# Kernel optimization log

Measured on AMD Instinct MI355X. Metric: run time of the kernel, lower is better.

## Reference

```python
import jax, jax.numpy as jnp
import numpy as np

B, T, D, U, M = 64, 512, 256, 512, 64  # batch, seq_len, input_dim, units, memory_size


def setup_inputs() -> dict:
    key = jax.random.key(0)
    ks = jax.random.split(key, 16)
    g = lambda k, s: (jax.random.normal(k, s, dtype=jnp.float32) * 0.05)
    return {
        "x": g(ks[0], (B, T, D)),
        "Wi": g(ks[1], (D, U)), "Ui": g(ks[2], (U, U)), "bi": jnp.zeros((U,), jnp.float32),
        "Wf": g(ks[3], (D, U)), "Uf": g(ks[4], (U, U)), "bf": jnp.ones((U,), jnp.float32),
        "Wo": g(ks[5], (D, U)), "Uo": g(ks[6], (U, U)), "bo": jnp.zeros((U,), jnp.float32),
        "Wc": g(ks[7], (D, U)), "Uc": g(ks[8], (U, U)), "bc": jnp.zeros((U,), jnp.float32),
        "We": g(ks[9], (D, M)), "Ue": g(ks[10], (U, M)), "be": jnp.zeros((M,), jnp.float32),
    }


def reference(x, Wi, Ui, bi, Wf, Uf, bf, Wo, Uo, bo, Wc, Uc, bc, We, Ue, be):
    # Fuse the 5 per-step input/hidden matmuls into single GEMMs (same math).
    Wcat = jnp.concatenate([Wi, Wf, Wo, Wc, We], axis=1)   # [D, 4U+M]
    Ucat = jnp.concatenate([Ui, Uf, Uo, Uc, Ue], axis=1)   # [U, 4U+M]
    bcat = jnp.concatenate([bi, bf, bo, bc, be], axis=0)   # [4U+M]

    def step(carry, x_t):
        h, mem = carry                                      # h:[B,U], mem:[B,M,U]
        z = x_t @ Wcat + h @ Ucat + bcat                    # [B, 4U+M]
        zi, zf, zo, zc, ze = jnp.split(z, [U, 2 * U, 3 * U, 4 * U], axis=-1)
        i = jax.nn.sigmoid(zi)
        f = jax.nn.sigmoid(zf)
        o = jax.nn.sigmoid(zo)
        c_tilde = jnp.tanh(zc)
        e = jax.nn.softmax(ze, axis=-1)                     # [B,M]
        mem_contrib = jnp.einsum('bm,bmu->bu', e, mem)      # softmax-weighted memory read
        c = f * mem_contrib + i * c_tilde
        h_new = o * jnp.tanh(c)
        mem_new = jnp.concatenate([c[:, None, :], mem[:, :-1, :]], axis=1)  # shift-register write
        return (h_new, mem_new), h_new

    h0 = jnp.zeros((B, U), x.dtype)
    m0 = jnp.zeros((B, M, U), x.dtype)
    (_, _), hs = jax.lax.scan(step, (h0, m0), jnp.swapaxes(x, 0, 1))  # hs:[T,B,U]
    return jnp.swapaxes(hs, 0, 1)                           # [B,T,U]
```

## Files before the change

### kernel.cpp

```cpp
#include <hip/hip_runtime.h>

#define Bn   64
#define Tn   512
#define Dn   256
#define Un   512
#define Mn   64
#define NTHR 256
#define GRID 128

#define HB_OFF    5120
#define BP_OFF    70656
#define BPU_SH    1572864
#define BPE_SH    49152
#define XF_OFF    881664
#define XF_U4     1048576
#define WS_NEED_F (XF_OFF + XF_U4*4)

typedef __attribute__((ext_vector_type(8))) short short8;
typedef __attribute__((ext_vector_type(4))) float f32x4;
typedef unsigned long long ull;

union frag8 { short8 s; f32x4 f; uint4 u; };

__device__ __forceinline__ float sigmoidf_(float v) { return 1.0f / (1.0f + __expf(-v)); }
__device__ __forceinline__ float tanhf_(float v) {
    const float e = __expf(2.0f * v);
    return (e - 1.0f) / (e + 1.0f);
}

__device__ __forceinline__ unsigned short f2bf(float f) {
    unsigned u = __float_as_uint(f);
    return (unsigned short)((u + 0x7FFFu + ((u >> 16) & 1u)) >> 16);
}

__device__ __forceinline__ void st_agent_u64(ull* p, ull v) {
    __hip_atomic_store(p, v, __ATOMIC_RELAXED, __HIP_MEMORY_SCOPE_AGENT);
}
__device__ __forceinline__ ull ld_agent_u64(const void* p) {
    return __hip_atomic_load((const ull*)p, __ATOMIC_RELAXED, __HIP_MEMORY_SCOPE_AGENT);
}

template<bool USEXF>
__global__ __launch_bounds__(NTHR, 1) void xlstm_k(
    const float* __restrict__ x,
    const float* __restrict__ bi, const float* __restrict__ bf_,
    const float* __restrict__ bo, const float* __restrict__ bc,
    const float* __restrict__ be,
    float* __restrict__ out, float* __restrict__ ws)
{
    __shared__ unsigned short sA[16 * 776];
    __shared__ float zs[1024];
    __shared__ float zel[16 * 68];
    __shared__ float esm[16 * 68];
    __shared__ float sbe[64];

    ull* hb64 = (ull*)(ws + HB_OFF);
    const unsigned short* BPU = (const unsigned short*)(ws + BP_OFF);
    const unsigned short* BPE = BPU + BPU_SH;
    const uint4* XFp = (const uint4*)(ws + XF_OFF);

    const int tid = threadIdx.x, wg = blockIdx.x;
    const int bt = wg >> 5, r = wg & 31;
    const int b0 = bt << 4, u0 = r << 4;
    const int lane = tid & 63, w = tid >> 6;
    const int quad = lane >> 4, m16 = lane & 15;
    const unsigned short* aBase = sA + m16 * 776 + (quad << 3);
    const uint4* xfb = XFp + ((ull)bt << 18) + lane;

    const int bb = tid >> 4, uu = tid & 15;
    const float bia_i = bi[u0 + uu], bia_f = bf_[u0 + uu];
    const float bia_o = bo[u0 + uu], bia_c = bc[u0 + uu];
    float* outp = out + (ull)((b0 + bb) * Tn) * 512 + u0 + uu;
    const float4* xg = (const float4*)x;

    if (tid < 64) sbe[tid] = be[tid];

    unsigned ch[32];
    #pragma unroll
    for (int j = 0; j < 32; ++j) ch[j] = 0u;

    const short8* Bg = (const short8*)BPU + (r * 4 + w) * 24 * 64 + lane;
    const short8* Be = (const short8*)BPE + w * 24 * 64 + lane;
    frag8 Bfg[24], Bfe[24];
    #pragma unroll
    for (int i = 0; i < 24; ++i) { Bfg[i].s = Bg[i << 6]; Bfe[i].s = Be[i << 6]; }

    frag8 xf[8];
    float4 xv[4];
    if (USEXF) {
        #pragma unroll
        for (int kb = 0; kb < 8; ++kb) xf[kb].u = xfb[kb << 6];
    } else {
        #pragma unroll
        for (int i2 = 0; i2 < 4; ++i2) {
            const int i = (i2 << 8) + tid;
            xv[i2] = xg[(((b0 + (i >> 6)) * Tn) << 6) + (i & 63)];
        }
        #pragma unroll
        for (int i2 = 0; i2 < 4; ++i2) {
            const int i = (i2 << 8) + tid;
            ushort4 o; o.x = f2bf(xv[i2].x); o.y = f2bf(xv[i2].y);
            o.z = f2bf(xv[i2].z); o.w = f2bf(xv[i2].w);
            *(ushort4*)(sA + (i >> 6) * 776 + ((i & 63) << 2)) = o;
        }
        #pragma unroll
        for (int i2 = 0; i2 < 4; ++i2) {
            const int i = (i2 << 8) + tid;
            xv[i2] = xg[(((b0 + (i >> 6)) * Tn + 1) << 6) + (i & 63)];
        }
    }
    __syncthreads();

    for (int t = 0; t < Tn; ++t) {
        #pragma unroll
        for (int i = 0; i < 24; ++i) {
            asm volatile("" : "+a"(Bfg[i].f));
            asm volatile("" : "+a"(Bfe[i].f));
        }

        f32x4 ag0 = {0.f, 0.f, 0.f, 0.f}, ag1 = ag0, ae0 = ag0, ae1 = ag0;
        #pragma unroll
        for (int kb = 0; kb < 8; kb += 2) {
            const short8 a0 = USEXF ? xf[kb].s     : *(const short8*)(aBase + (kb << 5));
            const short8 a1 = USEXF ? xf[kb + 1].s : *(const short8*)(aBase + ((kb + 1) << 5));
            ag0 = __builtin_amdgcn_mfma_f32_16x16x32_bf16(a0, Bfg[kb].s,     ag0, 0, 0, 0);
            ae0 = __builtin_amdgcn_mfma_f32_16x16x32_bf16(a0, Bfe[kb].s,     ae0, 0, 0, 0);
            ag1 = __builtin_amdgcn_mfma_f32_16x16x32_bf16(a1, Bfg[kb + 1].s, ag1, 0, 0, 0);
            ae1 = __builtin_amdgcn_mfma_f32_16x16x32_bf16(a1, Bfe[kb + 1].s, ae1, 0, 0, 0);
        }

        if (USEXF) {
            if (t + 1 < Tn) {
                const uint4* xn = xfb + ((t + 1) << 9);
                #pragma unroll
                for (int kb = 0; kb < 8; ++kb) xf[kb].u = xn[kb << 6];
            }
        }

        const ull* hp = hb64 + ((t & 1) << 14) + (b0 << 8) + tid;
        ull hv[16];
        #pragma unroll
        for (int j = 0; j < 16; ++j) hv[j] = ld_agent_u64(hp + (j << 8));
        {
            const unsigned want = (unsigned)t;
            while (true) {
                bool ok = true;
                #pragma unroll
                for (int j = 0; j < 16; ++j) ok &= ((unsigned)(hv[j] >> 32) == want);
                if (__all(ok)) break;
                __builtin_amdgcn_s_sleep(1);
                #pragma unroll
                for (int j = 0; j < 16; ++j) hv[j] = ld_agent_u64(hp + (j << 8));
            }
        }

        #pragma unroll
        for (int j = 0; j < 16; ++j)
            *(unsigned*)(sA + j * 776 + 256 + (tid << 1)) = (unsigned)hv[j];
        __syncthreads();

        if (!USEXF) {
            if (t + 1 < Tn) {
                #pragma unroll
                for (int i2 = 0; i2 < 4; ++i2) {
                    const int i = (i2 << 8) + tid;
                    ushort4 o; o.x = f2bf(xv[i2].x); o.y = f2bf(xv[i2].y);
                    o.z = f2bf(xv[i2].z); o.w = f2bf(xv[i2].w);
                    *(ushort4*)(sA + (i >> 6) * 776 + ((i & 63) << 2)) = o;
                }
            }
            if (t + 2 < Tn) {
                #pragma unroll
                for (int i2 = 0; i2 < 4; ++i2) {
                    const int i = (i2 << 8) + tid;
                    xv[i2] = xg[(((b0 + (i >> 6)) * Tn + t + 2) << 6) + (i & 63)];
                }
            }
        }

        #pragma unroll
        for (int kb = 8; kb < 24; kb += 2) {
            const short8 a0 = *(const short8*)(aBase + (kb << 5));
            const short8 a1 = *(const short8*)(aBase + ((kb + 1) << 5));
            ag0 = __builtin_amdgcn_mfma_f32_16x16x32_bf16(a0, Bfg[kb].s,     ag0, 0, 0, 0);
            ae0 = __builtin_amdgcn_mfma_f32_16x16x32_bf16(a0, Bfe[kb].s,     ae0, 0, 0, 0);
            ag1 = __builtin_amdgcn_mfma_f32_16x16x32_bf16(a1, Bfg[kb + 1].s, ag1, 0, 0, 0);
            ae1 = __builtin_amdgcn_mfma_f32_16x16x32_bf16(a1, Bfe[kb + 1].s, ae1, 0, 0, 0);
        }

        #pragma unroll
        for (int i = 0; i < 4; ++i) {
            zs[(((quad << 2) + i) * 16 + m16) * 4 + w] = ag0[i] + ag1[i];
            zel[((quad << 2) + i) * 68 + (w << 4) + m16] = ae0[i] + ae1[i];
        }
        __syncthreads();

        {
            const float* zb = zel + bb * 68;
            const int l = uu;
            const float e0 = __expf(zb[l]      + sbe[l]);
            const float e1 = __expf(zb[l + 16] + sbe[l + 16]);
            const float e2 = __expf(zb[l + 32] + sbe[l + 32]);
            const float e3 = __expf(zb[l + 48] + sbe[l + 48]);
            float ssum = (e0 + e1) + (e2 + e3);
            #pragma unroll
            for (int off = 8; off; off >>= 1) ssum += __shfl_xor(ssum, off, 16);
            const float inv = 1.0f / ssum;
            float* st = esm + bb * 68;
            st[l]      = e0 * inv;
            st[l + 16] = e1 * inv;
            st[l + 32] = e2 * inv;
            st[l + 48] = e3 * inv;
        }

        const float4 z4 = *(const float4*)(zs + (tid << 2));
        const float zi = z4.x + bia_i;
        const float zf = z4.y + bia_f;
        const float zo = z4.z + bia_o;
        const float zc = z4.w + bia_c;
        float mcA = 0.f, mcB = 0.f, mcC = 0.f, mcD = 0.f;
        const float4* ef = (const float4*)(esm + bb * 68);
        #pragma unroll
        for (int q = 0; q < 4; ++q) {
            const float4 e4 = ef[q];
            const unsigned c0 = ch[2 * q], c1 = ch[2 * q + 1];
            mcA = fmaf(__uint_as_float(c0 << 16),         e4.x, mcA);
            mcA = fmaf(__uint_as_float(c0 & 0xFFFF0000u), e4.y, mcA);
            mcA = fmaf(__uint_as_float(c1 << 16),         e4.z, mcA);
            mcA = fmaf(__uint_as_float(c1 & 0xFFFF0000u), e4.w, mcA);
        }
        #pragma unroll
        for (int q = 4; q < 8; ++q) {
            const float4 e4 = ef[q];
            const unsigned c0 = ch[2 * q], c1 = ch[2 * q + 1];
            mcB = fmaf(__uint_as_float(c0 << 16),         e4.x, mcB);
            mcB = fmaf(__uint_as_float(c0 & 0xFFFF0000u), e4.y, mcB);
            mcB = fmaf(__uint_as_float(c1 << 16),         e4.z, mcB);
            mcB = fmaf(__uint_as_float(c1 & 0xFFFF0000u), e4.w, mcB);
        }
        #pragma unroll
        for (int q = 8; q < 12; ++q) {
            const float4 e4 = ef[q];
            const unsigned c0 = ch[2 * q], c1 = ch[2 * q + 1];
            mcC = fmaf(__uint_as_float(c0 << 16),         e4.x, mcC);
            mcC = fmaf(__uint_as_float(c0 & 0xFFFF0000u), e4.y, mcC);
            mcC = fmaf(__uint_as_float(c1 << 16),         e4.z, mcC);
            mcC = fmaf(__uint_as_float(c1 & 0xFFFF0000u), e4.w, mcC);
        }
        #pragma unroll
        for (int q = 12; q < 16; ++q) {
            const float4 e4 = ef[q];
            const unsigned c0 = ch[2 * q], c1 = ch[2 * q + 1];
            mcD = fmaf(__uint_as_float(c0 << 16),         e4.x, mcD);
            mcD = fmaf(__uint_as_float(c0 & 0xFFFF0000u), e4.y, mcD);
            mcD = fmaf(__uint_as_float(c1 << 16),         e4.z, mcD);
            mcD = fmaf(__uint_as_float(c1 & 0xFFFF0000u), e4.w, mcD);
        }
        const float mc = (mcA + mcB) + (mcC + mcD);
        const float cc = sigmoidf_(zf) * mc + sigmoidf_(zi) * tanhf_(zc);
        const float hh = sigmoidf_(zo) * tanhf_(cc);
        const float nh = __shfl_xor(hh, 1);
        if (!(tid & 1)) {
            const ull v = ((ull)(unsigned)(t + 1) << 32)
                        | (ull)((unsigned)f2bf(hh) | ((unsigned)f2bf(nh) << 16));
            st_agent_u64(hb64 + (((t + 1) & 1) << 14) + ((b0 + bb) << 8)
                         + ((u0 + uu) >> 1), v);
        }
        outp[t << 9] = hh;

        #pragma unroll
        for (int j = 31; j > 0; --j) ch[j] = (ch[j] << 16) | (ch[j - 1] >> 16);
        ch[0] = (ch[0] << 16) | (unsigned)f2bf(cc);
    }
}

__global__ __launch_bounds__(NTHR) void init_k(
    const float* __restrict__ x,
    const float* __restrict__ Wi, const float* __restrict__ Ui,
    const float* __restrict__ Wf, const float* __restrict__ Uf,
    const float* __restrict__ Wo, const float* __restrict__ Uo,
    const float* __restrict__ Wc, const float* __restrict__ Uc,
    const float* __restrict__ We, const float* __restrict__ Ue,
    float* __restrict__ ws, int fillxf)
{
    const int idx = blockIdx.x * NTHR + threadIdx.x;
    const int stride = gridDim.x * NTHR;
    unsigned* ctr = (unsigned*)ws;
    for (int i = idx; i < 512; i += stride) ctr[i] = 0u;
    unsigned* hbu = (unsigned*)(ws + HB_OFF);
    for (int i = idx; i < 65536; i += stride) hbu[i] = 0u;

    unsigned short* BPU = (unsigned short*)(ws + BP_OFF);
    unsigned short* BPE = BPU + BPU_SH;
    const float* Wg[4] = {Wi, Wf, Wo, Wc};
    const float* Ug[4] = {Ui, Uf, Uo, Uc};
    for (int g = idx; g < 196608; g += stride) {
        const int lane = g & 63, rest = g >> 6;
        const int kb = rest % 24, rest2 = rest / 24;
        const int w2 = rest2 & 3, rr = rest2 >> 2;
        const int cs = (rr << 4) + (lane & 15);
        const int kbase = (kb << 5) + ((lane >> 4) << 3);
        #pragma unroll
        for (int j = 0; j < 8; ++j) {
            const int k = kbase + j;
            const float v = (k < 256) ? Wg[w2][(k << 9) + cs]
                                      : Ug[w2][((k - 256) << 9) + cs];
            BPU[(g << 3) + j] = f2bf(v);
        }
    }
    for (int g = idx; g < 6144; g += stride) {
        const int lane = g & 63, rest = g >> 6;
        const int kb = rest % 24, w2 = rest / 24;
        const int cs = (w2 << 4) + (lane & 15);
        const int kbase = (kb << 5) + ((lane >> 4) << 3);
        #pragma unroll
        for (int j = 0; j < 8; ++j) {
            const int k = kbase + j;
            const float v = (k < 256) ? We[(k << 6) + cs] : Ue[((k - 256) << 6) + cs];
            BPE[(g << 3) + j] = f2bf(v);
        }
    }
    if (fillxf) {
        uint4* XFp = (uint4*)(ws + XF_OFF);
        for (int g = idx; g < XF_U4; g += stride) {
            const int lane = g & 63, kb = (g >> 6) & 7, t = (g >> 9) & 511, bt = g >> 18;
            const int m16 = lane & 15, quad = lane >> 4;
            const int b = (bt << 4) + m16;
            const int k0 = (kb << 5) + (quad << 3);
            const float* xr = x + (((ull)(b * Tn + t)) << 8) + k0;
            unsigned short us[8];
            #pragma unroll
            for (int j = 0; j < 8; ++j) us[j] = f2bf(xr[j]);
            uint4 o;
            o.x = (unsigned)us[0] | ((unsigned)us[1] << 16);
            o.y = (unsigned)us[2] | ((unsigned)us[3] << 16);
            o.z = (unsigned)us[4] | ((unsigned)us[5] << 16);
            o.w = (unsigned)us[6] | ((unsigned)us[7] << 16);
            XFp[g] = o;
        }
    }
}

extern "C" void kernel_launch(void* const* d_in, const int* in_sizes, int n_in,
                              void* d_out, int out_size, void* d_ws, size_t ws_size,
                              hipStream_t stream) {
    const float* x  = (const float*)d_in[0];
    const float* Wi = (const float*)d_in[1];
    const float* Ui = (const float*)d_in[2];
    const float* bi = (const float*)d_in[3];
    const float* Wf = (const float*)d_in[4];
    const float* Uf = (const float*)d_in[5];
    const float* bf = (const float*)d_in[6];
    const float* Wo = (const float*)d_in[7];
    const float* Uo = (const float*)d_in[8];
    const float* bo = (const float*)d_in[9];
    const float* Wc = (const float*)d_in[10];
    const float* Uc = (const float*)d_in[11];
    const float* bc = (const float*)d_in[12];
    const float* We = (const float*)d_in[13];
    const float* Ue = (const float*)d_in[14];
    const float* be = (const float*)d_in[15];
    float* out = (float*)d_out;
    float* ws  = (float*)d_ws;

    const int use_xf = (ws_size >= (size_t)WS_NEED_F * sizeof(float)) ? 1 : 0;

    init_k<<<512, NTHR, 0, stream>>>(x, Wi, Ui, Wf, Uf, Wo, Uo, Wc, Uc, We, Ue,
                                     ws, use_xf);

    void* args[] = { &x, &bi, &bf, &bo, &bc, &be, &out, &ws };
    const void* kfun = use_xf ? (const void*)xlstm_k<true>
                              : (const void*)xlstm_k<false>;
    hipError_t e = hipLaunchCooperativeKernel(kfun, dim3(GRID), dim3(NTHR),
                                              args, 0, stream);
    if (e != hipSuccess) {
        (void)hipGetLastError();
        if (use_xf)
            xlstm_k<true><<<GRID, NTHR, 0, stream>>>(x, bi, bf, bo, bc, be, out, ws);
        else
            xlstm_k<false><<<GRID, NTHR, 0, stream>>>(x, bi, bf, bo, bc, be, out, ws);
    }
}
```

Measured before the change: 1.693 ms.

## Interleave two batch tiles per workgroup to hide recurrent sync latency

Adds a dual kernel in which each of 64 workgroups handles two independent 16-row batch tiles. While one tile waits on other workgroups' hidden-state flags, the other tile's input-projection MFMAs and gate math run. This is meant to hide the cross-workgroup spin-wait latency of the serial recurrence. In exchange, half as many CUs are used, and each workgroup does twice the per-step work and carries twice the register state (two memory shift registers and two x fragment sets).

After: 3.065 ms. 81.0% more time.

```diff
diff --git a/kernel.cpp b/kernel.cpp
--- a/kernel.cpp
+++ b/kernel.cpp
@@ -6,7 +6,8 @@
 #define Un   512
 #define Mn   64
 #define NTHR 256
-#define GRID 128
+#define GRID_DUAL 64
+#define GRID_SNG  128
 
 #define HB_OFF    5120
 #define BP_OFF    70656
@@ -40,7 +41,314 @@
     return __hip_atomic_load((const ull*)p, __ATOMIC_RELAXED, __HIP_MEMORY_SCOPE_AGENT);
 }
 
-template<bool USEXF>
+__global__ __launch_bounds__(NTHR, 1) void xlstm_dual(
+    const float* __restrict__ bi, const float* __restrict__ bf_,
+    const float* __restrict__ bo, const float* __restrict__ bc,
+    const float* __restrict__ be,
+    float* __restrict__ out, float* __restrict__ ws)
+{
+    __shared__ unsigned short sH[16 * 520];
+    __shared__ float zs[1024];
+    __shared__ float zel[16 * 68];
+    __shared__ float esm[16 * 68];
+    __shared__ float sbe[64];
+
+    ull* hb64 = (ull*)(ws + HB_OFF);
+    const unsigned short* BPU = (const unsigned short*)(ws + BP_OFF);
+    const unsigned short* BPE = BPU + BPU_SH;
+    const uint4* XFp = (const uint4*)(ws + XF_OFF);
+
+    const int tid = threadIdx.x, wg = blockIdx.x;
+    const int r = wg & 31, pr = wg >> 5;
+    const int btA = pr, btB = pr + 2;
+    const int b0A = btA << 4, b0B = btB << 4, u0 = r << 4;
+    const int lane = tid & 63, w = tid >> 6;
+    const int quad = lane >> 4, m16 = lane & 15;
+    const unsigned short* aBase = sH + m16 * 520 + (quad << 3);
+    const uint4* xfbA = XFp + ((ull)btA << 18) + lane;
+    const uint4* xfbB = XFp + ((ull)btB << 18) + lane;
+
+    const int bb = tid >> 4, uu = tid & 15;
+    const float bia_i = bi[u0 + uu], bia_f = bf_[u0 + uu];
+    const float bia_o = bo[u0 + uu], bia_c = bc[u0 + uu];
+    float* outpA = out + (ull)((b0A + bb) * Tn) * 512 + u0 + uu;
+    float* outpB = out + (ull)((b0B + bb) * Tn) * 512 + u0 + uu;
+
+    if (tid < 64) sbe[tid] = be[tid];
+
+    unsigned chA[32], chB[32];
+    #pragma unroll
+    for (int j = 0; j < 32; ++j) { chA[j] = 0u; chB[j] = 0u; }
+
+    const short8* Bg = (const short8*)BPU + (r * 4 + w) * 24 * 64 + lane;
+    const short8* Be = (const short8*)BPE + w * 24 * 64 + lane;
+    frag8 Bfg[24], Bfe[24];
+    #pragma unroll
+    for (int i = 0; i < 24; ++i) { Bfg[i].s = Bg[i << 6]; Bfe[i].s = Be[i << 6]; }
+
+    frag8 xfA[8], xfB[8];
+    #pragma unroll
+    for (int kb = 0; kb < 8; ++kb) { xfA[kb].u = xfbA[kb << 6]; xfB[kb].u = xfbB[kb << 6]; }
+
+    ull hv[16];
+    {
+        const ull* hp = hb64 + (b0A << 8) + tid;
+        #pragma unroll
+        for (int j = 0; j < 16; ++j) hv[j] = ld_agent_u64(hp + (j << 8));
+    }
+    __syncthreads();
+
+    for (int t = 0; t < Tn; ++t) {
+        #pragma unroll
+        for (int i = 0; i < 24; ++i) {
+            asm volatile("" : "+a"(Bfg[i].f));
+            asm volatile("" : "+a"(Bfe[i].f));
+        }
+        const unsigned want = (unsigned)t;
+        const ull* hpA = hb64 + ((t & 1) << 14) + (b0A << 8) + tid;
+        const ull* hpB = hb64 + ((t & 1) << 14) + (b0B << 8) + tid;
+
+        f32x4 agA0 = {0.f,0.f,0.f,0.f}, agA1 = agA0, aeA0 = agA0, aeA1 = agA0;
+        f32x4 agB0 = agA0, agB1 = agA0, aeB0 = agA0, aeB1 = agA0;
+        #pragma unroll
+        for (int kb = 0; kb < 8; kb += 2) {
+            agA0 = __builtin_amdgcn_mfma_f32_16x16x32_bf16(xfA[kb].s,     Bfg[kb].s,     agA0, 0, 0, 0);
+            aeA0 = __builtin_amdgcn_mfma_f32_16x16x32_bf16(xfA[kb].s,     Bfe[kb].s,     aeA0, 0, 0, 0);
+            agA1 = __builtin_amdgcn_mfma_f32_16x16x32_bf16(xfA[kb + 1].s, Bfg[kb + 1].s, agA1, 0, 0, 0);
+            aeA1 = __builtin_amdgcn_mfma_f32_16x16x32_bf16(xfA[kb + 1].s, Bfe[kb + 1].s, aeA1, 0, 0, 0);
+        }
+        #pragma unroll
+        for (int kb = 0; kb < 8; kb += 2) {
+            agB0 = __builtin_amdgcn_mfma_f32_16x16x32_bf16(xfB[kb].s,     Bfg[kb].s,     agB0, 0, 0, 0);
+            aeB0 = __builtin_amdgcn_mfma_f32_16x16x32_bf16(xfB[kb].s,     Bfe[kb].s,     aeB0, 0, 0, 0);
+            agB1 = __builtin_amdgcn_mfma_f32_16x16x32_bf16(xfB[kb + 1].s, Bfg[kb + 1].s, agB1, 0, 0, 0);
+            aeB1 = __builtin_amdgcn_mfma_f32_16x16x32_bf16(xfB[kb + 1].s, Bfe[kb + 1].s, aeB1, 0, 0, 0);
+        }
+
+        while (true) {
+            bool ok = true;
+            #pragma unroll
+            for (int j = 0; j < 16; ++j) ok &= ((unsigned)(hv[j] >> 32) == want);
+            if (__all(ok)) break;
+            __builtin_amdgcn_s_sleep(1);
+            #pragma unroll
+            for (int j = 0; j < 16; ++j) hv[j] = ld_agent_u64(hpA + (j << 8));
+        }
+        #pragma unroll
+        for (int j = 0; j < 16; ++j)
+            *(unsigned*)(sH + j * 520 + (tid << 1)) = (unsigned)hv[j];
+        __syncthreads();
+
+        #pragma unroll
+        for (int j = 0; j < 16; ++j) hv[j] = ld_agent_u64(hpB + (j << 8));
+
+        #pragma unroll
+        for (int kb = 8; kb < 24; kb += 2) {
+            const short8 a0 = *(const short8*)(aBase + ((kb - 8) << 5));
+            const short8 a1 = *(const short8*)(aBase + ((kb - 7) << 5));
+            agA0 = __builtin_amdgcn_mfma_f32_16x16x32_bf16(a0, Bfg[kb].s,     agA0, 0, 0, 0);
+            aeA0 = __builtin_amdgcn_mfma_f32_16x16x32_bf16(a0, Bfe[kb].s,     aeA0, 0, 0, 0);
+            agA1 = __builtin_amdgcn_mfma_f32_16x16x32_bf16(a1, Bfg[kb + 1].s, agA1, 0, 0, 0);
+            aeA1 = __builtin_amdgcn_mfma_f32_16x16x32_bf16(a1, Bfe[kb + 1].s, aeA1, 0, 0, 0);
+        }
+        #pragma unroll
+        for (int i = 0; i < 4; ++i) {
+            zs[(((quad << 2) + i) * 16 + m16) * 4 + w] = agA0[i] + agA1[i];
+            zel[((quad << 2) + i) * 68 + (w << 4) + m16] = aeA0[i] + aeA1[i];
+        }
+        __syncthreads();
+
+        {
+            const float* zb = zel + bb * 68;
+            const int l = uu;
+            const float e0 = __expf(zb[l]      + sbe[l]);
+            const float e1 = __expf(zb[l + 16] + sbe[l + 16]);
+            const float e2 = __expf(zb[l + 32] + sbe[l + 32]);
+            const float e3 = __expf(zb[l + 48] + sbe[l + 48]);
+            float ssum = (e0 + e1) + (e2 + e3);
+            #pragma unroll
+            for (int off = 8; off; off >>= 1) ssum += __shfl_xor(ssum, off, 16);
+            const float inv = 1.0f / ssum;
+            float* st = esm + bb * 68;
+            st[l] = e0 * inv; st[l + 16] = e1 * inv;
+            st[l + 32] = e2 * inv; st[l + 48] = e3 * inv;
+        }
+        {
+            const float4 z4 = *(const float4*)(zs + (tid << 2));
+            const float zi = z4.x + bia_i, zf = z4.y + bia_f;
+            const float zo = z4.z + bia_o, zc = z4.w + bia_c;
+            float mcA = 0.f, mcB2 = 0.f, mcC = 0.f, mcD = 0.f;
+            const float4* ef = (const float4*)(esm + bb * 68);
+            #pragma unroll
+            for (int q = 0; q < 4; ++q) {
+                const float4 e4 = ef[q];
+                const unsigned c0 = chA[2 * q], c1 = chA[2 * q + 1];
+                mcA = fmaf(__uint_as_float(c0 << 16),         e4.x, mcA);
+                mcA = fmaf(__uint_as_float(c0 & 0xFFFF0000u), e4.y, mcA);
+                mcA = fmaf(__uint_as_float(c1 << 16),         e4.z, mcA);
+                mcA = fmaf(__uint_as_float(c1 & 0xFFFF0000u), e4.w, mcA);
+            }
+            #pragma unroll
+            for (int q = 4; q < 8; ++q) {
+                const float4 e4 = ef[q];
+                const unsigned c0 = chA[2 * q], c1 = chA[2 * q + 1];
+                mcB2 = fmaf(__uint_as_float(c0 << 16),         e4.x, mcB2);
+                mcB2 = fmaf(__uint_as_float(c0 & 0xFFFF0000u), e4.y, mcB2);
+                mcB2 = fmaf(__uint_as_float(c1 << 16),         e4.z, mcB2);
+                mcB2 = fmaf(__uint_as_float(c1 & 0xFFFF0000u), e4.w, mcB2);
+            }
+            #pragma unroll
+            for (int q = 8; q < 12; ++q) {
+                const float4 e4 = ef[q];
+                const unsigned c0 = chA[2 * q], c1 = chA[2 * q + 1];
+                mcC = fmaf(__uint_as_float(c0 << 16),         e4.x, mcC);
+                mcC = fmaf(__uint_as_float(c0 & 0xFFFF0000u), e4.y, mcC);
+                mcC = fmaf(__uint_as_float(c1 << 16),         e4.z, mcC);
+                mcC = fmaf(__uint_as_float(c1 & 0xFFFF0000u), e4.w, mcC);
+            }
+            #pragma unroll
+            for (int q = 12; q < 16; ++q) {
+                const float4 e4 = ef[q];
+                const unsigned c0 = chA[2 * q], c1 = chA[2 * q + 1];
+                mcD = fmaf(__uint_as_float(c0 << 16),         e4.x, mcD);
+                mcD = fmaf(__uint_as_float(c0 & 0xFFFF0000u), e4.y, mcD);
+                mcD = fmaf(__uint_as_float(c1 << 16),         e4.z, mcD);
+                mcD = fmaf(__uint_as_float(c1 & 0xFFFF0000u), e4.w, mcD);
+            }
+            const float mc = (mcA + mcB2) + (mcC + mcD);
+            const float cc = sigmoidf_(zf) * mc + sigmoidf_(zi) * tanhf_(zc);
+            const float hh = sigmoidf_(zo) * tanhf_(cc);
+            const float nh = __shfl_xor(hh, 1);
+            if (!(tid & 1)) {
+                const ull v = ((ull)(unsigned)(t + 1) << 32)
+                            | (ull)((unsigned)f2bf(hh) | ((unsigned)f2bf(nh) << 16));
+                st_agent_u64(hb64 + (((t + 1) & 1) << 14) + ((b0A + bb) << 8)
+                             + ((u0 + uu) >> 1), v);
+            }
+            outpA[t << 9] = hh;
+            #pragma unroll
+            for (int j = 31; j > 0; --j) chA[j] = (chA[j] << 16) | (chA[j - 1] >> 16);
+            chA[0] = (chA[0] << 16) | (unsigned)f2bf(cc);
+        }
+
+        while (true) {
+            bool ok = true;
+            #pragma unroll
+            for (int j = 0; j < 16; ++j) ok &= ((unsigned)(hv[j] >> 32) == want);
+            if (__all(ok)) break;
+            __builtin_amdgcn_s_sleep(1);
+            #pragma unroll
+            for (int j = 0; j < 16; ++j) hv[j] = ld_agent_u64(hpB + (j << 8));
+        }
+        #pragma unroll
+        for (int j = 0; j < 16; ++j)
+            *(unsigned*)(sH + j * 520 + (tid << 1)) = (unsigned)hv[j];
+        __syncthreads();
+
+        if (t + 1 < Tn) {
+            const uint4* xnA = xfbA + ((t + 1) << 9);
+            const uint4* xnB = xfbB + ((t + 1) << 9);
+            #pragma unroll
+            for (int kb = 0; kb < 8; ++kb) { xfA[kb].u = xnA[kb << 6]; xfB[kb].u = xnB[kb << 6]; }
+        }
+
+        #pragma unroll
+        for (int kb = 8; kb < 24; kb += 2) {
+            const short8 a0 = *(const short8*)(aBase + ((kb - 8) << 5));
+            const short8 a1 = *(const short8*)(aBase + ((kb - 7) << 5));
+            agB0 = __builtin_amdgcn_mfma_f32_16x16x32_bf16(a0, Bfg[kb].s,     agB0, 0, 0, 0);
+            aeB0 = __builtin_amdgcn_mfma_f32_16x16x32_bf16(a0, Bfe[kb].s,     aeB0, 0, 0, 0);
+            agB1 = __builtin_amdgcn_mfma_f32_16x16x32_bf16(a1, Bfg[kb + 1].s, agB1, 0, 0, 0);
+            aeB1 = __builtin_amdgcn_mfma_f32_16x16x32_bf16(a1, Bfe[kb + 1].s, aeB1, 0, 0, 0);
+        }
+        #pragma unroll
+        for (int i = 0; i < 4; ++i) {
+            zs[(((quad << 2) + i) * 16 + m16) * 4 + w] = agB0[i] + agB1[i];
+            zel[((quad << 2) + i) * 68 + (w << 4) + m16] = aeB0[i] + aeB1[i];
+        }
+        __syncthreads();
+
+        {
+            const float* zb = zel + bb * 68;
+            const int l = uu;
+            const float e0 = __expf(zb[l]      + sbe[l]);
+            const float e1 = __expf(zb[l + 16] + sbe[l + 16]);
+            const float e2 = __expf(zb[l + 32] + sbe[l + 32]);
+            const float e3 = __expf(zb[l + 48] + sbe[l + 48]);
+            float ssum = (e0 + e1) + (e2 + e3);
+            #pragma unroll
+            for (int off = 8; off; off >>= 1) ssum += __shfl_xor(ssum, off, 16);
+            const float inv = 1.0f / ssum;
+            float* st = esm + bb * 68;
+            st[l] = e0 * inv; st[l + 16] = e1 * inv;
+            st[l + 32] = e2 * inv; st[l + 48] = e3 * inv;
+        }
+        {
+            const float4 z4 = *(const float4*)(zs + (tid << 2));
+            const float zi = z4.x + bia_i, zf = z4.y + bia_f;
+            const float zo = z4.z + bia_o, zc = z4.w + bia_c;
+            float mcA = 0.f, mcB2 = 0.f, mcC = 0.f, mcD = 0.f;
+            const float4* ef = (const float4*)(esm + bb * 68);
+            #pragma unroll
+            for (int q = 0; q < 4; ++q) {
+                const float4 e4 = ef[q];
+                const unsigned c0 = chB[2 * q], c1 = chB[2 * q + 1];
+                mcA = fmaf(__uint_as_float(c0 << 16),         e4.x, mcA);
+                mcA = fmaf(__uint_as_float(c0 & 0xFFFF0000u), e4.y, mcA);
+                mcA = fmaf(__uint_as_float(c1 << 16),         e4.z, mcA);
+                mcA = fmaf(__uint_as_float(c1 & 0xFFFF0000u), e4.w, mcA);
+            }
+            #pragma unroll
+            for (int q = 4; q < 8; ++q) {
+                const float4 e4 = ef[q];
+                const unsigned c0 = chB[2 * q], c1 = chB[2 * q + 1];
+                mcB2 = fmaf(__uint_as_float(c0 << 16),         e4.x, mcB2);
+                mcB2 = fmaf(__uint_as_float(c0 & 0xFFFF0000u), e4.y, mcB2);
+                mcB2 = fmaf(__uint_as_float(c1 << 16),         e4.z, mcB2);
+                mcB2 = fmaf(__uint_as_float(c1 & 0xFFFF0000u), e4.w, mcB2);
+            }
+            #pragma unroll
+            for (int q = 8; q < 12; ++q) {
+                const float4 e4 = ef[q];
+                const unsigned c0 = chB[2 * q], c1 = chB[2 * q + 1];
+                mcC = fmaf(__uint_as_float(c0 << 16),         e4.x, mcC);
+                mcC = fmaf(__uint_as_float(c0 & 0xFFFF0000u), e4.y, mcC);
+                mcC = fmaf(__uint_as_float(c1 << 16),         e4.z, mcC);
+                mcC = fmaf(__uint_as_float(c1 & 0xFFFF0000u), e4.w, mcC);
+            }
+            #pragma unroll
+            for (int q = 12; q < 16; ++q) {
+                const float4 e4 = ef[q];
+                const unsigned c0 = chB[2 * q], c1 = chB[2 * q + 1];
+                mcD = fmaf(__uint_as_float(c0 << 16),         e4.x, mcD);
+                mcD = fmaf(__uint_as_float(c0 & 0xFFFF0000u), e4.y, mcD);
+                mcD = fmaf(__uint_as_float(c1 << 16),         e4.z, mcD);
+                mcD = fmaf(__uint_as_float(c1 & 0xFFFF0000u), e4.w, mcD);
+            }
+            const float mc = (mcA + mcB2) + (mcC + mcD);
+            const float cc = sigmoidf_(zf) * mc + sigmoidf_(zi) * tanhf_(zc);
+            const float hh = sigmoidf_(zo) * tanhf_(cc);
+            const float nh = __shfl_xor(hh, 1);
+            if (!(tid & 1)) {
+                const ull v = ((ull)(unsigned)(t + 1) << 32)
+                            | (ull)((unsigned)f2bf(hh) | ((unsigned)f2bf(nh) << 16));
+                st_agent_u64(hb64 + (((t + 1) & 1) << 14) + ((b0B + bb) << 8)
+                             + ((u0 + uu) >> 1), v);
+            }
+            outpB[t << 9] = hh;
+            #pragma unroll
+            for (int j = 31; j > 0; --j) chB[j] = (chB[j] << 16) | (chB[j - 1] >> 16);
+            chB[0] = (chB[0] << 16) | (unsigned)f2bf(cc);
+        }
+
+        if (t + 1 < Tn) {
+            const ull* hn = hb64 + (((t + 1) & 1) << 14) + (b0A << 8) + tid;
+            #pragma unroll
+            for (int j = 0; j < 16; ++j) hv[j] = ld_agent_u64(hn + (j << 8));
+        }
+    }
+}
+
 __global__ __launch_bounds__(NTHR, 1) void xlstm_k(
     const float* __restrict__ x,
     const float* __restrict__ bi, const float* __restrict__ bf_,
@@ -57,7 +365,6 @@
     ull* hb64 = (ull*)(ws + HB_OFF);
     const unsigned short* BPU = (const unsigned short*)(ws + BP_OFF);
     const unsigned short* BPE = BPU + BPU_SH;
-    const uint4* XFp = (const uint4*)(ws + XF_OFF);
 
     const int tid = threadIdx.x, wg = blockIdx.x;
     const int bt = wg >> 5, r = wg & 31;
@@ -65,7 +372,6 @@
     const int lane = tid & 63, w = tid >> 6;
     const int quad = lane >> 4, m16 = lane & 15;
     const unsigned short* aBase = sA + m16 * 776 + (quad << 3);
-    const uint4* xfb = XFp + ((ull)bt << 18) + lane;
 
     const int bb = tid >> 4, uu = tid & 15;
     const float bia_i = bi[u0 + uu], bia_f = bf_[u0 + uu];
@@ -74,7 +380,6 @@
     const float4* xg = (const float4*)x;
 
     if (tid < 64) sbe[tid] = be[tid];
-
     unsigned ch[32];
     #pragma unroll
     for (int j = 0; j < 32; ++j) ch[j] = 0u;
@@ -85,29 +390,23 @@
     #pragma unroll
     for (int i = 0; i < 24; ++i) { Bfg[i].s = Bg[i << 6]; Bfe[i].s = Be[i << 6]; }
 
-    frag8 xf[8];
     float4 xv[4];
-    if (USEXF) {
-        #pragma unroll
-        for (int kb = 0; kb < 8; ++kb) xf[kb].u = xfb[kb << 6];
-    } else {
-        #pragma unroll
-        for (int i2 = 0; i2 < 4; ++i2) {
-            const int i = (i2 << 8) + tid;
-            xv[i2] = xg[(((b0 + (i >> 6)) * Tn) << 6) + (i & 63)];
-        }
-        #pragma unroll
-        for (int i2 = 0; i2 < 4; ++i2) {
-            const int i = (i2 << 8) + tid;
-            ushort4 o; o.x = f2bf(xv[i2].x); o.y = f2bf(xv[i2].y);
-            o.z = f2bf(xv[i2].z); o.w = f2bf(xv[i2].w);
-            *(ushort4*)(sA + (i >> 6) * 776 + ((i & 63) << 2)) = o;
-        }
-        #pragma unroll
-        for (int i2 = 0; i2 < 4; ++i2) {
-            const int i = (i2 << 8) + tid;
-            xv[i2] = xg[(((b0 + (i >> 6)) * Tn + 1) << 6) + (i & 63)];
-        }
+    #pragma unroll
+    for (int i2 = 0; i2 < 4; ++i2) {
+        const int i = (i2 << 8) + tid;
+        xv[i2] = xg[(((b0 + (i >> 6)) * Tn) << 6) + (i & 63)];
+    }
+    #pragma unroll
+    for (int i2 = 0; i2 < 4; ++i2) {
+        const int i = (i2 << 8) + tid;
+        ushort4 o; o.x = f2bf(xv[i2].x); o.y = f2bf(xv[i2].y);
+        o.z = f2bf(xv[i2].z); o.w = f2bf(xv[i2].w);
+        *(ushort4*)(sA + (i >> 6) * 776 + ((i & 63) << 2)) = o;
+    }
+    #pragma unroll
+    for (int i2 = 0; i2 < 4; ++i2) {
+        const int i = (i2 << 8) + tid;
+        xv[i2] = xg[(((b0 + (i >> 6)) * Tn + 1) << 6) + (i & 63)];
     }
     __syncthreads();
 
@@ -117,26 +416,16 @@
             asm volatile("" : "+a"(Bfg[i].f));
             asm volatile("" : "+a"(Bfe[i].f));
         }
-
         f32x4 ag0 = {0.f, 0.f, 0.f, 0.f}, ag1 = ag0, ae0 = ag0, ae1 = ag0;
         #pragma unroll
         for (int kb = 0; kb < 8; kb += 2) {
-            const short8 a0 = USEXF ? xf[kb].s     : *(const short8*)(aBase + (kb << 5));
-            const short8 a1 = USEXF ? xf[kb + 1].s : *(const short8*)(aBase + ((kb + 1) << 5));
+            const short8 a0 = *(const short8*)(aBase + (kb << 5));
+            const short8 a1 = *(const short8*)(aBase + ((kb + 1) << 5));
             ag0 = __builtin_amdgcn_mfma_f32_16x16x32_bf16(a0, Bfg[kb].s,     ag0, 0, 0, 0);
             ae0 = __builtin_amdgcn_mfma_f32_16x16x32_bf16(a0, Bfe[kb].s,     ae0, 0, 0, 0);
             ag1 = __builtin_amdgcn_mfma_f32_16x16x32_bf16(a1, Bfg[kb + 1].s, ag1, 0, 0, 0);
             ae1 = __builtin_amdgcn_mfma_f32_16x16x32_bf16(a1, Bfe[kb + 1].s, ae1, 0, 0, 0);
         }
-
-        if (USEXF) {
-            if (t + 1 < Tn) {
-                const uint4* xn = xfb + ((t + 1) << 9);
-                #pragma unroll
-                for (int kb = 0; kb < 8; ++kb) xf[kb].u = xn[kb << 6];
-            }
-        }
-
         const ull* hp = hb64 + ((t & 1) << 14) + (b0 << 8) + tid;
         ull hv[16];
         #pragma unroll
@@ -153,31 +442,27 @@
                 for (int j = 0; j < 16; ++j) hv[j] = ld_agent_u64(hp + (j << 8));
             }
         }
-
         #pragma unroll
         for (int j = 0; j < 16; ++j)
             *(unsigned*)(sA + j * 776 + 256 + (tid << 1)) = (unsigned)hv[j];
         __syncthreads();
 
-        if (!USEXF) {
-            if (t + 1 < Tn) {
-                #pragma unroll
-                for (int i2 = 0; i2 < 4; ++i2) {
-                    const int i = (i2 << 8) + tid;
-                    ushort4 o; o.x = f2bf(xv[i2].x); o.y = f2bf(xv[i2].y);
-                    o.z = f2bf(xv[i2].z); o.w = f2bf(xv[i2].w);
-                    *(ushort4*)(sA + (i >> 6) * 776 + ((i & 63) << 2)) = o;
-                }
-            }
-            if (t + 2 < Tn) {
-                #pragma unroll
-                for (int i2 = 0; i2 < 4; ++i2) {
-                    const int i = (i2 << 8) + tid;
-                    xv[i2] = xg[(((b0 + (i >> 6)) * Tn + t + 2) << 6) + (i & 63)];
-                }
-            }
-        }
-
+        if (t + 1 < Tn) {
+            #pragma unroll
+            for (int i2 = 0; i2 < 4; ++i2) {
+                const int i = (i2 << 8) + tid;
+                ushort4 o; o.x = f2bf(xv[i2].x); o.y = f2bf(xv[i2].y);
+                o.z = f2bf(xv[i2].z); o.w = f2bf(xv[i2].w);
+                *(ushort4*)(sA + (i >> 6) * 776 + ((i & 63) << 2)) = o;
+            }
+        }
+        if (t + 2 < Tn) {
+            #pragma unroll
+            for (int i2 = 0; i2 < 4; ++i2) {
+                const int i = (i2 << 8) + tid;
+                xv[i2] = xg[(((b0 + (i >> 6)) * Tn + t + 2) << 6) + (i & 63)];
+            }
+        }
         #pragma unroll
         for (int kb = 8; kb < 24; kb += 2) {
             const short8 a0 = *(const short8*)(aBase + (kb << 5));
@@ -187,14 +472,12 @@
             ag1 = __builtin_amdgcn_mfma_f32_16x16x32_bf16(a1, Bfg[kb + 1].s, ag1, 0, 0, 0);
             ae1 = __builtin_amdgcn_mfma_f32_16x16x32_bf16(a1, Bfe[kb + 1].s, ae1, 0, 0, 0);
         }
-
         #pragma unroll
         for (int i = 0; i < 4; ++i) {
             zs[(((quad << 2) + i) * 16 + m16) * 4 + w] = ag0[i] + ag1[i];
             zel[((quad << 2) + i) * 68 + (w << 4) + m16] = ae0[i] + ae1[i];
         }
         __syncthreads();
-
         {
             const float* zb = zel + bb * 68;
             const int l = uu;
@@ -207,17 +490,12 @@
             for (int off = 8; off; off >>= 1) ssum += __shfl_xor(ssum, off, 16);
             const float inv = 1.0f / ssum;
             float* st = esm + bb * 68;
-            st[l]      = e0 * inv;
-            st[l + 16] = e1 * inv;
-            st[l + 32] = e2 * inv;
-            st[l + 48] = e3 * inv;
-        }
-
+            st[l] = e0 * inv; st[l + 16] = e1 * inv;
+            st[l + 32] = e2 * inv; st[l + 48] = e3 * inv;
+        }
         const float4 z4 = *(const float4*)(zs + (tid << 2));
-        const float zi = z4.x + bia_i;
-        const float zf = z4.y + bia_f;
-        const float zo = z4.z + bia_o;
-        const float zc = z4.w + bia_c;
+        const float zi = z4.x + bia_i, zf = z4.y + bia_f;
+        const float zo = z4.z + bia_o, zc = z4.w + bia_c;
         float mcA = 0.f, mcB = 0.f, mcC = 0.f, mcD = 0.f;
         const float4* ef = (const float4*)(esm + bb * 68);
         #pragma unroll
@@ -267,7 +545,6 @@
                          + ((u0 + uu) >> 1), v);
         }
         outp[t << 9] = hh;
-
         #pragma unroll
         for (int j = 31; j > 0; --j) ch[j] = (ch[j] << 16) | (ch[j - 1] >> 16);
         ch[0] = (ch[0] << 16) | (unsigned)f2bf(cc);
@@ -368,16 +645,23 @@
     init_k<<<512, NTHR, 0, stream>>>(x, Wi, Ui, Wf, Uf, Wo, Uo, Wc, Uc, We, Ue,
                                      ws, use_xf);
 
-    void* args[] = { &x, &bi, &bf, &bo, &bc, &be, &out, &ws };
-    const void* kfun = use_xf ? (const void*)xlstm_k<true>
-                              : (const void*)xlstm_k<false>;
-    hipError_t e = hipLaunchCooperativeKernel(kfun, dim3(GRID), dim3(NTHR),
-                                              args, 0, stream);
-    if (e != hipSuccess) {
-        (void)hipGetLastError();
-        if (use_xf)
-            xlstm_k<true><<<GRID, NTHR, 0, stream>>>(x, bi, bf, bo, bc, be, out, ws);
-        else
-            xlstm_k<false><<<GRID, NTHR, 0, stream>>>(x, bi, bf, bo, bc, be, out, ws);
-    }
-}
+    if (use_xf) {
+        void* args[] = { &bi, &bf, &bo, &bc, &be, &out, &ws };
+        hipError_t e = hipLaunchCooperativeKernel((const void*)xlstm_dual,
+                                                  dim3(GRID_DUAL), dim3(NTHR),
+                                                  args, 0, stream);
+        if (e != hipSuccess) {
+            (void)hipGetLastError();
+            xlstm_dual<<<GRID_DUAL, NTHR, 0, stream>>>(bi, bf, bo, bc, be, out, ws);
+        }
+    } else {
+        void* args[] = { &x, &bi, &bf, &bo, &bc, &be, &out, &ws };
+        hipError_t e = hipLaunchCooperativeKernel((const void*)xlstm_k,
+                                                  dim3(GRID_SNG), dim3(NTHR),
+                                                  args, 0, stream);
+        if (e != hipSuccess) {
+            (void)hipGetLastError();
+            xlstm_k<<<GRID_SNG, NTHR, 0, stream>>>(x, bi, bf, bo, bc, be, out, ws);
+        }
+    }
+}
```
